# Performance work log

Measured on AMD Instinct MI355X. Metric: run time of the kernel, lower is better.

Reference implementation:

```python
import jax, jax.numpy as jnp
import numpy as np

B, T, H, K = 64, 512, 768, 32


def setup_inputs() -> dict:
    key = jax.random.key(0)
    ks = jax.random.split(key, 6)
    x = jax.random.normal(ks[0], (B, T, H), jnp.float32)
    y = jax.random.randint(ks[1], (B, T), 0, K)
    sequence_lengths = jax.random.randint(ks[2], (B,), 1, T + 1)
    W = jax.random.normal(ks[3], (H, K), jnp.float32) * 0.02
    b = jnp.zeros((K,), jnp.float32)
    transition_params = jax.random.normal(ks[4], (K, K), jnp.float32) * 0.1
    return dict(x=x, y=y, sequence_lengths=sequence_lengths, W=W, b=b,
                transition_params=transition_params)


def _crf_log_norm(pot, lengths, trans):
    # pot: [B,T,K]; forward algorithm with per-example length masking
    alpha0 = pot[:, 0]
    def step(alpha, inp):
        pot_t, t = inp
        new = jax.nn.logsumexp(alpha[:, :, None] + trans[None], axis=1) + pot_t
        keep = (t < lengths)[:, None]
        return jnp.where(keep, new, alpha), None
    xs = (jnp.swapaxes(pot[:, 1:], 0, 1), jnp.arange(1, pot.shape[1]))
    alpha, _ = jax.lax.scan(step, alpha0, xs)
    return jax.nn.logsumexp(alpha, axis=-1)  # [B]


def _crf_sequence_score(pot, y, lengths, trans):
    t_idx = jnp.arange(pot.shape[1])
    mask_u = (t_idx[None, :] < lengths[:, None]).astype(pot.dtype)      # [B,T]
    unary = jnp.take_along_axis(pot, y[..., None], axis=2)[..., 0]      # [B,T]
    unary = jnp.sum(unary * mask_u, axis=1)
    mask_b = (t_idx[None, :-1] < (lengths - 1)[:, None]).astype(pot.dtype)
    binary = trans[y[:, :-1], y[:, 1:]]                                 # [B,T-1]
    binary = jnp.sum(binary * mask_b, axis=1)
    return unary + binary


def _crf_decode(pot, lengths, trans):
    Bb, Tt, Kk = pot.shape
    alpha0 = pot[:, 0]
    ident = jnp.broadcast_to(jnp.arange(Kk), (Bb, Kk))
    def fwd(alpha, inp):
        pot_t, t = inp
        scores = alpha[:, :, None] + trans[None]   # [B,K,K] prev->cur
        bp = jnp.argmax(scores, axis=1)            # [B,K]
        new = jnp.max(scores, axis=1) + pot_t
        keep = (t < lengths)[:, None]
        alpha = jnp.where(keep, new, alpha)
        bp = jnp.where(keep, bp, ident)            # identity past end of seq
        return alpha, bp
    xs = (jnp.swapaxes(pot[:, 1:], 0, 1), jnp.arange(1, Tt))
    alpha, bps = jax.lax.scan(fwd, alpha0, xs)     # bps: [T-1,B,K]
    last = jnp.argmax(alpha, axis=-1)              # [B]
    def back(tag, bp):
        prev = jnp.take_along_axis(bp, tag[:, None], axis=1)[:, 0]
        return prev, prev
    _, prevs = jax.lax.scan(back, last, bps, reverse=True)  # [T-1,B]
    tags = jnp.concatenate([prevs, last[None]], axis=0).T   # [B,T]
    return tags


def reference(x, y, sequence_lengths, W, b, transition_params):
    pot = jnp.einsum('bth,hk->btk', x, W) + b      # dense projection to tag space
    log_likelihood = (_crf_sequence_score(pot, y, sequence_lengths, transition_params)
                      - _crf_log_norm(pot, sequence_lengths, transition_params))
    preds = _crf_decode(pot, sequence_lengths, transition_params)
    mask = (jnp.arange(pot.shape[1])[None, :] < sequence_lengths[:, None]).astype(preds.dtype)
    preds = preds * mask
    return log_likelihood, preds
```

## Files before the change

kernel.cpp:

```cpp
#include <hip/hip_runtime.h>
#include <hip/hip_bf16.h>
#include <stdint.h>


#define TT 512
#define KK 32
#define HH 768
#define NB 64

#define WS_POT 0
#define WS_VA  4198400
#define WS_BP  8396800
#define WS_LOGZ 9445376
#define WS_LAST 9445632

template <int CTRL>
__device__ __forceinline__ float dppx(float x) {
  return __int_as_float(__builtin_amdgcn_update_dpp(
      0, __float_as_int(x), CTRL, 0xF, 0xF, true));
}

typedef unsigned int uint2v __attribute__((ext_vector_type(2)));

#if __has_builtin(__builtin_amdgcn_permlane16_swap)
__device__ __forceinline__ float xor16f(float x) {
  const unsigned xu = __float_as_uint(x);
  const uint2v q = __builtin_amdgcn_permlane16_swap(xu, xu, false, false);
  return __uint_as_float(q.x ^ q.y ^ xu);
}
#else
__device__ __forceinline__ float xor16f(float x) {
  return __int_as_float(__builtin_amdgcn_ds_swizzle(__float_as_int(x), 0x401F));
}
#endif

#if __has_builtin(__builtin_amdgcn_permlane32_swap)
__device__ __forceinline__ float xor32f(float x) {
  const unsigned xu = __float_as_uint(x);
  const uint2v q = __builtin_amdgcn_permlane32_swap(xu, xu, false, false);
  return __uint_as_float(q.x ^ q.y ^ xu);
}
#else
__device__ __forceinline__ float xor32f(float x) { return __shfl_xor(x, 32, 64); }
#endif

__device__ __forceinline__ float redmax32(float v) {
  v = fmaxf(v, dppx<0xB1>(v));
  v = fmaxf(v, dppx<0x4E>(v));
  v = fmaxf(v, dppx<0x141>(v));
  v = fmaxf(v, dppx<0x128>(v));
  v = fmaxf(v, xor16f(v));
  return v;
}
__device__ __forceinline__ float redsum32(float v) {
  v += dppx<0xB1>(v);
  v += dppx<0x4E>(v);
  v += dppx<0x141>(v);
  v += dppx<0x128>(v);
  v += xor16f(v);
  return v;
}

__device__ __forceinline__ int gmap(int m) {
  return ((m & 1) ? 1 : 0) ^ ((m & 2) ? 2 : 0) ^ ((m & 4) ? 7 : 0) ^ ((m & 8) ? 8 : 0);
}

#define REPL_TREE(A)                                            \
  A[1] = dppx<0xB1>(A[0]);                                      \
  _Pragma("unroll") for (int p = 0; p < 2; ++p) A[2 + p] = dppx<0x4E>(A[p]);  \
  _Pragma("unroll") for (int p = 0; p < 4; ++p) A[4 + p] = dppx<0x141>(A[p]); \
  _Pragma("unroll") for (int p = 0; p < 8; ++p) A[8 + p] = dppx<0x128>(A[p]);

__global__ __launch_bounds__(256) void gemm_pot(const float* __restrict__ x,
                                                const float* __restrict__ W,
                                                const float* __restrict__ bias,
                                                float* __restrict__ pot) {
  __shared__ float4 xs4[64][16];
  __shared__ float4 wt4[32][16];
  const int tid = threadIdx.x;
  const int row0 = blockIdx.x * 64;
  const int cg = tid & 15;
  const int rg = tid >> 4;
  const int c0 = cg * 2;
  float acc[4][2] = {{0.f, 0.f}, {0.f, 0.f}, {0.f, 0.f}, {0.f, 0.f}};

  for (int h0 = 0; h0 < HH; h0 += 64) {
#pragma unroll
    for (int p = 0; p < 4; ++p) {
      const int fi = tid + p * 256;
      const int r = fi >> 4, s = fi & 15;
      const float4 v = *(const float4*)(&x[(size_t)(row0 + r) * HH + h0 + s * 4]);
      xs4[r][s ^ ((r >> 2) & 3)] = v;
    }
    {
      const int c = tid & 31;
      const int hb = (tid >> 5) * 8;
      float* wf = (float*)(&wt4[0][0]);
#pragma unroll
      for (int i2 = 0; i2 < 8; ++i2) {
        const int hh = hb + i2;
        const int slot = (hh >> 2) ^ ((c >> 1) & 15);
        wf[c * 64 + slot * 4 + (hh & 3)] = W[(size_t)(h0 + hh) * KK + c];
      }
    }
    __syncthreads();
#pragma unroll
    for (int s = 0; s < 16; ++s) {
      float4 xv[4];
#pragma unroll
      for (int i = 0; i < 4; ++i) xv[i] = xs4[rg * 4 + i][s ^ (rg & 3)];
      const float4 wv0 = wt4[c0][s ^ cg];
      const float4 wv1 = wt4[c0 + 1][s ^ cg];
#pragma unroll
      for (int i = 0; i < 4; ++i) {
        acc[i][0] += xv[i].x * wv0.x + xv[i].y * wv0.y + xv[i].z * wv0.z + xv[i].w * wv0.w;
        acc[i][1] += xv[i].x * wv1.x + xv[i].y * wv1.y + xv[i].z * wv1.z + xv[i].w * wv1.w;
      }
    }
    __syncthreads();
  }
#pragma unroll
  for (int i = 0; i < 4; ++i) {
    const int row = row0 + rg * 4 + i;
    float2 o = make_float2(acc[i][0] + bias[c0], acc[i][1] + bias[c0 + 1]);
    *(float2*)(&pot[(size_t)row * KK + c0]) = o;
  }
}

__global__ __launch_bounds__(64) void scan2(const float* __restrict__ pot,
                                            const int* __restrict__ lens,
                                            const float* __restrict__ trans,
                                            float* __restrict__ va,
                                            float* __restrict__ logZ,
                                            int* __restrict__ last) {
  const int lane = threadIdx.x;
  const int k = lane & 31;
  const int jh = lane >> 5;
  const bool is_lse = (blockIdx.x < 64);
  const int b = is_lse ? blockIdx.x : blockIdx.x - 64;
  const int len = lens[b];
  const float* pp = pot + (size_t)b * (TT * KK) + k;

  if (is_lse) {
    float etrx[16];
#pragma unroll
    for (int m = 0; m < 16; ++m)
      etrx[m] = __expf(trans[((k ^ gmap(m) ^ (jh << 4)) << 5) + k]);
    const float a0 = pp[0];
    const float M0 = redmax32(a0);
    float a = __expf(a0 - M0);
    float alog = M0;
    float ep[8], en[8];
#pragma unroll
    for (int i = 0; i < 8; ++i) ep[i] = __expf(pp[(size_t)(1 + i) * KK]);
    for (int tb = 1; tb < len; tb += 8) {
#pragma unroll
      for (int i = 0; i < 8; ++i) en[i] = pp[(size_t)(tb + 8 + i) * KK];
#pragma unroll
      for (int i = 0; i < 8; ++i) {
        const int t = tb + i;
        if (t >= len) break;
        float A[16];
        const float u16 = xor16f(a);
        A[0] = jh ? u16 : a;
        REPL_TREE(A)
        float d0 = 0.f, d1 = 0.f, d2 = 0.f, d3 = 0.f;
#pragma unroll
        for (int p = 0; p < 4; ++p) {
          d0 += A[4 * p + 0] * etrx[4 * p + 0];
          d1 += A[4 * p + 1] * etrx[4 * p + 1];
          d2 += A[4 * p + 2] * etrx[4 * p + 2];
          d3 += A[4 * p + 3] * etrx[4 * p + 3];
        }
        float part = (d0 + d1) + (d2 + d3);
        a = (part + xor32f(part)) * ep[i];
        if ((t & 3) == 0) {
          const float mx = redmax32(a);
          alog += __logf(mx);
          a *= (1.0f / mx);
        }
      }
#pragma unroll
      for (int i = 0; i < 8; ++i) ep[i] = __expf(en[i]);
    }
    const float ssum = redsum32(a);
    if (lane == 0) logZ[b] = alog + __logf(ssum);
  } else {
    float trx[16];
#pragma unroll
    for (int m = 0; m < 16; ++m)
      trx[m] = trans[((k ^ gmap(m) ^ (jh << 4)) << 5) + k];
    float a = pp[0];
    float* vap = va + (size_t)b * (TT * KK) + k;
    if (lane < 32) vap[0] = a;
    float pb[8], pn[8];
#pragma unroll
    for (int i = 0; i < 8; ++i) pb[i] = pp[(size_t)(1 + i) * KK];
    for (int tb = 1; tb < len; tb += 8) {
#pragma unroll
      for (int i = 0; i < 8; ++i) pn[i] = pp[(size_t)(tb + 8 + i) * KK];
#pragma unroll
      for (int i = 0; i < 8; ++i) {
        const int t = tb + i;
        if (t >= len) break;
        float A[16];
        const float u16 = xor16f(a);
        A[0] = jh ? u16 : a;
        REPL_TREE(A)
        float s_[16];
#pragma unroll
        for (int m = 0; m < 16; ++m) s_[m] = A[m] + trx[m];
        const float m0 = fmaxf(fmaxf(s_[0], s_[1]), fmaxf(s_[2], s_[3]));
        const float m1 = fmaxf(fmaxf(s_[4], s_[5]), fmaxf(s_[6], s_[7]));
        const float m2 = fmaxf(fmaxf(s_[8], s_[9]), fmaxf(s_[10], s_[11]));
        const float m3 = fmaxf(fmaxf(s_[12], s_[13]), fmaxf(s_[14], s_[15]));
        const float part = fmaxf(fmaxf(m0, m1), fmaxf(m2, m3));
        a = fmaxf(part, xor32f(part)) + pb[i];
        if (lane < 32) vap[(size_t)t * KK] = a;
      }
#pragma unroll
      for (int i = 0; i < 8; ++i) pb[i] = pn[i];
    }
    float v = a;
    int idx = k;
#pragma unroll
    for (int mm = 16; mm >= 1; mm >>= 1) {
      const float vo = __shfl_xor(v, mm, 32);
      const int io = __shfl_xor(idx, mm, 32);
      if (vo > v || (vo == v && io < idx)) { v = vo; idx = io; }
    }
    if (lane == 0) last[b] = idx;
  }
}

__global__ __launch_bounds__(256) void bp_extract(const float* __restrict__ va,
                                                  const float* __restrict__ trans,
                                                  unsigned char* __restrict__ bp) {
  const int b = blockIdx.x >> 3;
  const int tbase = (blockIdx.x & 7) * 64;
  const int k = threadIdx.x & 31;
  const int ts = threadIdx.x >> 5;
  float tr[32];
#pragma unroll
  for (int j = 0; j < 32; ++j) tr[j] = trans[j * KK + k];
#pragma unroll
  for (int it = 0; it < 8; ++it) {
    const int t = tbase + it * 8 + ts;
    if (t < 1) continue;
    const float* row = va + ((size_t)b * TT + (t - 1)) * KK;
    float best = row[0] + tr[0];
    int bi = 0;
#pragma unroll
    for (int j = 1; j < 32; ++j) {
      const float s = row[j] + tr[j];
      if (s > best) { best = s; bi = j; }
    }
    bp[((size_t)b * TT + t) * KK + k] = (unsigned char)bi;
  }
}

__global__ __launch_bounds__(256) void backtrace_kernel(
    const unsigned char* __restrict__ bp, const int* __restrict__ lens,
    const int* __restrict__ last, const float* __restrict__ pot,
    const int* __restrict__ y, const float* __restrict__ trans,
    const float* __restrict__ logZ, float* __restrict__ out) {
  __shared__ unsigned char Ls[32736];
  __shared__ unsigned char sA[512], sB[512];
  __shared__ float red[256];
  const int b = blockIdx.x, tid = threadIdx.x;
  const int len = lens[b];

  for (int i = tid; i < TT * KK; i += 256) {
    const int t = i >> 5, k = i & 31;
    Ls[i] = (t >= 1 && t < len) ? bp[((size_t)b * TT + t) * KK + k] : (unsigned char)k;
  }
  __syncthreads();

  int off_prev = 0, cnt = 512;
  for (int l = 1; l <= 9; ++l) {
    const int off = 32 * (1024 - (1024 >> l));
    const int n = cnt >> 1;
    for (int i = tid; i < n * 32; i += 256) {
      const int m = i >> 5, k = i & 31;
      const int inner = Ls[off_prev + (2 * m + 1) * 32 + k];
      Ls[off + i] = Ls[off_prev + (2 * m) * 32 + inner];
    }
    __syncthreads();
    off_prev = off;
    cnt = n;
  }

  if (tid == 0) sA[0] = (unsigned char)last[b];
  __syncthreads();

  unsigned char* cur = sA;
  unsigned char* nxt = sB;
  int c2 = 1;
  for (int l = 9; l >= 1; --l) {
    const int offm = 32 * (1024 - (1024 >> (l - 1)));
    for (int i = tid; i < c2; i += 256) {
      const unsigned char s = cur[i];
      nxt[2 * i + 1] = s;
      nxt[2 * i] = Ls[offm + (2 * i + 1) * 32 + s];
    }
    __syncthreads();
    unsigned char* tmp = cur; cur = nxt; nxt = tmp;
    c2 <<= 1;
  }

  for (int t = tid; t < TT; t += 256)
    out[NB + (size_t)b * TT + t] = (t < len) ? (float)cur[t] : 0.f;

  float acc = 0.f;
  for (int t = tid; t < TT; t += 256) {
    const int yt = y[b * TT + t];
    if (t < len) acc += pot[((size_t)b * TT + t) * KK + yt];
    if (t < len - 1) acc += trans[yt * KK + y[b * TT + t + 1]];
  }
  red[tid] = acc;
  __syncthreads();
  for (int s = 128; s >= 1; s >>= 1) {
    if (tid < s) red[tid] += red[tid + s];
    __syncthreads();
  }
  if (tid == 0) out[b] = red[0] - logZ[b];
}

extern "C" void kernel_launch(void* const* d_in, const int* in_sizes, int n_in,
                              void* d_out, int out_size, void* d_ws, size_t ws_size,
                              hipStream_t stream) {
  const float* x = (const float*)d_in[0];
  const int* y = (const int*)d_in[1];
  const int* lens = (const int*)d_in[2];
  const float* W = (const float*)d_in[3];
  const float* bias = (const float*)d_in[4];
  const float* trans = (const float*)d_in[5];
  float* out = (float*)d_out;
  char* ws = (char*)d_ws;
  float* pot = (float*)(ws + WS_POT);
  float* va = (float*)(ws + WS_VA);
  unsigned char* bp = (unsigned char*)(ws + WS_BP);
  float* logZ = (float*)(ws + WS_LOGZ);
  int* last = (int*)(ws + WS_LAST);

  gemm_pot<<<512, 256, 0, stream>>>(x, W, bias, pot);
  scan2<<<128, 64, 0, stream>>>(pot, lens, trans, va, logZ, last);
  bp_extract<<<512, 256, 0, stream>>>(va, trans, bp);
  backtrace_kernel<<<64, 256, 0, stream>>>(bp, lens, last, pot, y, trans, logZ, out);
}
```

Measured before the change: 153.9 us.

## Interleave four sequences per wavefront in the CRF forward and Viterbi scans

The scan kernel now gives each 64-lane block four batch sequences instead of one, and advances their recurrences together in one time loop. The grid shrinks from 128 to 32 blocks. The goal is to hide the latency of the serial DPP and FMA chain in each step by overlapping four independent dependency chains. In exchange, each step does four times the work in a single wave and loops to the longest of the four lengths. Finished sequences are held with a select, and the Viterbi path now also writes va entries past each sequence's length. The scaling reciprocal is also swapped for a hardware rcp.

Result: slower. 337.7 us (+119.5%).

```diff
diff --git a/kernel.cpp b/kernel.cpp
--- a/kernel.cpp
+++ b/kernel.cpp
@@ -70,6 +70,39 @@
   _Pragma("unroll") for (int p = 0; p < 2; ++p) A[2 + p] = dppx<0x4E>(A[p]);  \
   _Pragma("unroll") for (int p = 0; p < 4; ++p) A[4 + p] = dppx<0x141>(A[p]); \
   _Pragma("unroll") for (int p = 0; p < 8; ++p) A[8 + p] = dppx<0x128>(A[p]);
+
+__device__ __forceinline__ float repl_dot(float a, const float* etrx, int jh) {
+  float A[16];
+  const float u16 = xor16f(a);
+  A[0] = jh ? u16 : a;
+  REPL_TREE(A)
+  float d0 = 0.f, d1 = 0.f, d2 = 0.f, d3 = 0.f;
+#pragma unroll
+  for (int p = 0; p < 4; ++p) {
+    d0 += A[4 * p + 0] * etrx[4 * p + 0];
+    d1 += A[4 * p + 1] * etrx[4 * p + 1];
+    d2 += A[4 * p + 2] * etrx[4 * p + 2];
+    d3 += A[4 * p + 3] * etrx[4 * p + 3];
+  }
+  float part = (d0 + d1) + (d2 + d3);
+  return part + xor32f(part);
+}
+
+__device__ __forceinline__ float repl_maxplus(float a, const float* trx, int jh) {
+  float A[16];
+  const float u16 = xor16f(a);
+  A[0] = jh ? u16 : a;
+  REPL_TREE(A)
+  float s_[16];
+#pragma unroll
+  for (int m = 0; m < 16; ++m) s_[m] = A[m] + trx[m];
+  const float m0 = fmaxf(fmaxf(s_[0], s_[1]), fmaxf(s_[2], s_[3]));
+  const float m1 = fmaxf(fmaxf(s_[4], s_[5]), fmaxf(s_[6], s_[7]));
+  const float m2 = fmaxf(fmaxf(s_[8], s_[9]), fmaxf(s_[10], s_[11]));
+  const float m3 = fmaxf(fmaxf(s_[12], s_[13]), fmaxf(s_[14], s_[15]));
+  const float part = fmaxf(fmaxf(m0, m1), fmaxf(m2, m3));
+  return fmaxf(part, xor32f(part));
+}
 
 __global__ __launch_bounds__(256) void gemm_pot(const float* __restrict__ x,
                                                 const float* __restrict__ W,
@@ -127,7 +160,7 @@
   }
 }
 
-__global__ __launch_bounds__(64) void scan2(const float* __restrict__ pot,
+__global__ __launch_bounds__(64) void scan4(const float* __restrict__ pot,
                                             const int* __restrict__ lens,
                                             const float* __restrict__ trans,
                                             float* __restrict__ va,
@@ -136,100 +169,121 @@
   const int lane = threadIdx.x;
   const int k = lane & 31;
   const int jh = lane >> 5;
-  const bool is_lse = (blockIdx.x < 64);
-  const int b = is_lse ? blockIdx.x : blockIdx.x - 64;
-  const int len = lens[b];
-  const float* pp = pot + (size_t)b * (TT * KK) + k;
+  const bool is_lse = (blockIdx.x < 16);
+  const int b0 = (is_lse ? blockIdx.x : blockIdx.x - 16) * 4;
+
+  int len[4];
+#pragma unroll
+  for (int q = 0; q < 4; ++q) len[q] = lens[b0 + q];
+  const int maxlen = max(max(len[0], len[1]), max(len[2], len[3]));
+  const float* pp[4];
+#pragma unroll
+  for (int q = 0; q < 4; ++q) pp[q] = pot + (size_t)(b0 + q) * (TT * KK) + k;
 
   if (is_lse) {
     float etrx[16];
 #pragma unroll
     for (int m = 0; m < 16; ++m)
       etrx[m] = __expf(trans[((k ^ gmap(m) ^ (jh << 4)) << 5) + k]);
-    const float a0 = pp[0];
-    const float M0 = redmax32(a0);
-    float a = __expf(a0 - M0);
-    float alog = M0;
-    float ep[8], en[8];
-#pragma unroll
-    for (int i = 0; i < 8; ++i) ep[i] = __expf(pp[(size_t)(1 + i) * KK]);
-    for (int tb = 1; tb < len; tb += 8) {
-#pragma unroll
-      for (int i = 0; i < 8; ++i) en[i] = pp[(size_t)(tb + 8 + i) * KK];
+    float a[4], alog[4];
+#pragma unroll
+    for (int q = 0; q < 4; ++q) {
+      const float a0 = pp[q][0];
+      const float M0 = redmax32(a0);
+      a[q] = __expf(a0 - M0);
+      alog[q] = M0;
+    }
+    float ep[4][8], en[4][8];
+#pragma unroll
+    for (int q = 0; q < 4; ++q)
+#pragma unroll
+      for (int i = 0; i < 8; ++i) ep[q][i] = __expf(pp[q][(size_t)(1 + i) * KK]);
+
+    for (int tb = 1; tb < maxlen; tb += 8) {
+#pragma unroll
+      for (int q = 0; q < 4; ++q)
+#pragma unroll
+        for (int i = 0; i < 8; ++i) en[q][i] = pp[q][(size_t)(tb + 8 + i) * KK];
 #pragma unroll
       for (int i = 0; i < 8; ++i) {
         const int t = tb + i;
-        if (t >= len) break;
-        float A[16];
-        const float u16 = xor16f(a);
-        A[0] = jh ? u16 : a;
-        REPL_TREE(A)
-        float d0 = 0.f, d1 = 0.f, d2 = 0.f, d3 = 0.f;
-#pragma unroll
-        for (int p = 0; p < 4; ++p) {
-          d0 += A[4 * p + 0] * etrx[4 * p + 0];
-          d1 += A[4 * p + 1] * etrx[4 * p + 1];
-          d2 += A[4 * p + 2] * etrx[4 * p + 2];
-          d3 += A[4 * p + 3] * etrx[4 * p + 3];
+        if (t >= maxlen) break;
+#pragma unroll
+        for (int q = 0; q < 4; ++q) {
+          const float anew = repl_dot(a[q], etrx, jh) * ep[q][i];
+          a[q] = (t < len[q]) ? anew : a[q];
         }
-        float part = (d0 + d1) + (d2 + d3);
-        a = (part + xor32f(part)) * ep[i];
         if ((t & 3) == 0) {
-          const float mx = redmax32(a);
-          alog += __logf(mx);
-          a *= (1.0f / mx);
+#pragma unroll
+          for (int q = 0; q < 4; ++q) {
+            const float mx = redmax32(a[q]);
+            alog[q] += __logf(mx);
+            a[q] *= __builtin_amdgcn_rcpf(mx);
+          }
         }
       }
 #pragma unroll
-      for (int i = 0; i < 8; ++i) ep[i] = __expf(en[i]);
-    }
-    const float ssum = redsum32(a);
-    if (lane == 0) logZ[b] = alog + __logf(ssum);
+      for (int q = 0; q < 4; ++q)
+#pragma unroll
+        for (int i = 0; i < 8; ++i) ep[q][i] = __expf(en[q][i]);
+    }
+#pragma unroll
+    for (int q = 0; q < 4; ++q) {
+      const float ssum = redsum32(a[q]);
+      if (lane == 0) logZ[b0 + q] = alog[q] + __logf(ssum);
+    }
   } else {
     float trx[16];
 #pragma unroll
     for (int m = 0; m < 16; ++m)
       trx[m] = trans[((k ^ gmap(m) ^ (jh << 4)) << 5) + k];
-    float a = pp[0];
-    float* vap = va + (size_t)b * (TT * KK) + k;
-    if (lane < 32) vap[0] = a;
-    float pb[8], pn[8];
-#pragma unroll
-    for (int i = 0; i < 8; ++i) pb[i] = pp[(size_t)(1 + i) * KK];
-    for (int tb = 1; tb < len; tb += 8) {
-#pragma unroll
-      for (int i = 0; i < 8; ++i) pn[i] = pp[(size_t)(tb + 8 + i) * KK];
+    float a[4];
+    float* vap[4];
+#pragma unroll
+    for (int q = 0; q < 4; ++q) {
+      a[q] = pp[q][0];
+      vap[q] = va + (size_t)(b0 + q) * (TT * KK) + k;
+      if (lane < 32) vap[q][0] = a[q];
+    }
+    float pb[4][8], pn[4][8];
+#pragma unroll
+    for (int q = 0; q < 4; ++q)
+#pragma unroll
+      for (int i = 0; i < 8; ++i) pb[q][i] = pp[q][(size_t)(1 + i) * KK];
+
+    for (int tb = 1; tb < maxlen; tb += 8) {
+#pragma unroll
+      for (int q = 0; q < 4; ++q)
+#pragma unroll
+        for (int i = 0; i < 8; ++i) pn[q][i] = pp[q][(size_t)(tb + 8 + i) * KK];
 #pragma unroll
       for (int i = 0; i < 8; ++i) {
         const int t = tb + i;
-        if (t >= len) break;
-        float A[16];
-        const float u16 = xor16f(a);
-        A[0] = jh ? u16 : a;
-        REPL_TREE(A)
-        float s_[16];
-#pragma unroll
-        for (int m = 0; m < 16; ++m) s_[m] = A[m] + trx[m];
-        const float m0 = fmaxf(fmaxf(s_[0], s_[1]), fmaxf(s_[2], s_[3]));
-        const float m1 = fmaxf(fmaxf(s_[4], s_[5]), fmaxf(s_[6], s_[7]));
-        const float m2 = fmaxf(fmaxf(s_[8], s_[9]), fmaxf(s_[10], s_[11]));
-        const float m3 = fmaxf(fmaxf(s_[12], s_[13]), fmaxf(s_[14], s_[15]));
-        const float part = fmaxf(fmaxf(m0, m1), fmaxf(m2, m3));
-        a = fmaxf(part, xor32f(part)) + pb[i];
-        if (lane < 32) vap[(size_t)t * KK] = a;
+        if (t >= maxlen) break;
+#pragma unroll
+        for (int q = 0; q < 4; ++q) {
+          const float anew = repl_maxplus(a[q], trx, jh) + pb[q][i];
+          a[q] = (t < len[q]) ? anew : a[q];
+          if (lane < 32) vap[q][(size_t)t * KK] = a[q];
+        }
       }
 #pragma unroll
-      for (int i = 0; i < 8; ++i) pb[i] = pn[i];
-    }
-    float v = a;
-    int idx = k;
-#pragma unroll
-    for (int mm = 16; mm >= 1; mm >>= 1) {
-      const float vo = __shfl_xor(v, mm, 32);
-      const int io = __shfl_xor(idx, mm, 32);
-      if (vo > v || (vo == v && io < idx)) { v = vo; idx = io; }
-    }
-    if (lane == 0) last[b] = idx;
+      for (int q = 0; q < 4; ++q)
+#pragma unroll
+        for (int i = 0; i < 8; ++i) pb[q][i] = pn[q][i];
+    }
+#pragma unroll
+    for (int q = 0; q < 4; ++q) {
+      float v = a[q];
+      int idx = k;
+#pragma unroll
+      for (int mm = 16; mm >= 1; mm >>= 1) {
+        const float vo = __shfl_xor(v, mm, 32);
+        const int io = __shfl_xor(idx, mm, 32);
+        if (vo > v || (vo == v && io < idx)) { v = vo; idx = io; }
+      }
+      if (lane == 0) last[b0 + q] = idx;
+    }
   }
 }
 
@@ -344,7 +398,7 @@
   int* last = (int*)(ws + WS_LAST);
 
   gemm_pot<<<512, 256, 0, stream>>>(x, W, bias, pot);
-  scan2<<<128, 64, 0, stream>>>(pot, lens, trans, va, logZ, last);
+  scan4<<<32, 64, 0, stream>>>(pot, lens, trans, va, logZ, last);
   bp_extract<<<512, 256, 0, stream>>>(va, trans, bp);
   backtrace_kernel<<<64, 256, 0, stream>>>(bp, lens, last, pot, y, trans, logZ, out);
 }
```
